# Optimization experiments

Hardware: AMD Instinct MI355X
Metric: run time of the kernel (lower is better)

Reference implementation:

```python
import jax, jax.numpy as jnp
import numpy as np

B, T_MEM, T_TGT = 32, 256, 128
E = H = 512          # embed_size == hidden_size == memory feature dim (required by module math)
V = 10000            # vocab size


def setup_inputs() -> dict:
    key = jax.random.key(0)
    ks = jax.random.split(key, 10)
    s = 0.05
    return {
        "memory": jax.random.normal(ks[0], (B, T_MEM, E), dtype=jnp.float32),
        "tgt": jax.random.randint(ks[1], (B, T_TGT), 0, V),
        "emb_in": jax.random.normal(ks[2], (V, E), dtype=jnp.float32) * s,
        "W_ih": jax.random.normal(ks[3], (4 * H, E + H), dtype=jnp.float32) * s,
        "W_hh": jax.random.normal(ks[4], (4 * H, H), dtype=jnp.float32) * s,
        "b_ih": jax.random.normal(ks[5], (4 * H,), dtype=jnp.float32) * s,
        "b_hh": jax.random.normal(ks[6], (4 * H,), dtype=jnp.float32) * s,
        "W_out": jax.random.normal(ks[7], (V, H), dtype=jnp.float32) * s,
        "b_out": jax.random.normal(ks[8], (V,), dtype=jnp.float32) * s,
    }


def reference(memory, tgt, emb_in, W_ih, W_hh, b_ih, b_hh, W_out, b_out):
    # memory: (B, T_mem, E); tgt: (B, T_tgt) int
    Bq, Tm, Ed = memory.shape
    Hd = W_hh.shape[1]
    scale = 1.0 / jnp.sqrt(jnp.asarray(Ed, dtype=memory.dtype))

    x_emb = emb_in[tgt]                       # (B, T_tgt, E) teacher-forced inputs
    x_seq = jnp.swapaxes(x_emb, 0, 1)         # (T_tgt, B, E) for scan

    def step(carry, x_t):
        h, c = carry                          # (B, H), (B, H)
        # scaled dot-product attention: query=h, keys=values=memory
        scores = jnp.einsum('be,bte->bt', h, memory) * scale
        attn = jax.nn.softmax(scores, axis=-1)
        context = jnp.einsum('bt,bte->be', attn, memory)   # (B, E)
        inp = jnp.concatenate([context, x_t], axis=-1)     # (B, E + E_embed)
        gates = inp @ W_ih.T + b_ih + h @ W_hh.T + b_hh    # (B, 4H)
        i, f, g, o = jnp.split(gates, 4, axis=-1)          # torch LSTMCell gate order
        c_new = jax.nn.sigmoid(f) * c + jax.nn.sigmoid(i) * jnp.tanh(g)
        h_new = jax.nn.sigmoid(o) * jnp.tanh(c_new)
        logits = h_new @ W_out.T + b_out                   # (B, V)
        return (h_new, c_new), logits

    h0 = jnp.zeros((Bq, Hd), dtype=memory.dtype)
    c0 = jnp.zeros((Bq, Hd), dtype=memory.dtype)
    _, logits_seq = jax.lax.scan(step, (h0, c0), x_seq)    # (T_tgt, B, V)
    return jnp.swapaxes(logits_seq, 0, 1)                  # (B, T_tgt, V)
```

## Files before the change

kernel.cpp:

```cpp
#include <hip/hip_runtime.h>
#include <stdint.h>

#define TT 128

typedef __attribute__((ext_vector_type(8))) short short8;
typedef __attribute__((ext_vector_type(4))) float f32x4;
typedef __attribute__((ext_vector_type(4))) uint32_t u32x4;

__device__ __forceinline__ float blo(uint32_t u){ union{uint32_t i; float f;} v; v.i = u << 16; return v.f; }
__device__ __forceinline__ float bhi(uint32_t u){ union{uint32_t i; float f;} v; v.i = u & 0xffff0000u; return v.f; }
__device__ __forceinline__ float bf2f(uint16_t u){ union{uint32_t i; float f;} v; v.i = ((uint32_t)u) << 16; return v.f; }
__device__ __forceinline__ uint16_t f2bf(float f){
  union{float f; uint32_t i;} v; v.f = f;
  uint32_t r = v.i + 0x7fffu + ((v.i >> 16) & 1u);
  return (uint16_t)(r >> 16);
}
__device__ __forceinline__ uint32_t bfpack(float a, float b) {
  return (uint32_t)f2bf(a) | ((uint32_t)f2bf(b) << 16);
}
__device__ __forceinline__ void xstore(uint32_t* p, uint32_t v) {
  __hip_atomic_store(p, v, __ATOMIC_RELAXED, __HIP_MEMORY_SCOPE_AGENT);
}
__device__ __forceinline__ uint32_t xload(const uint32_t* p) {
  return __hip_atomic_load(p, __ATOMIC_RELAXED, __HIP_MEMORY_SCOPE_AGENT);
}
__device__ __forceinline__ void xstore64(unsigned long long* p, unsigned long long v) {
  __hip_atomic_store(p, v, __ATOMIC_RELAXED, __HIP_MEMORY_SCOPE_AGENT);
}
__device__ __forceinline__ unsigned long long xload64(const unsigned long long* p) {
  return __hip_atomic_load(p, __ATOMIC_RELAXED, __HIP_MEMORY_SCOPE_AGENT);
}
__device__ __forceinline__ void xstoref(float* p, float v) {
  __hip_atomic_store(p, v, __ATOMIC_RELAXED, __HIP_MEMORY_SCOPE_AGENT);
}
__device__ __forceinline__ float xloadf(const float* p) {
  return __hip_atomic_load(p, __ATOMIC_RELAXED, __HIP_MEMORY_SCOPE_AGENT);
}

__global__ __launch_bounds__(256) void k_prep_mem(const float* __restrict__ mem,
                                                  uint32_t* __restrict__ memK,
                                                  uint32_t* __restrict__ memT) {
  int idx = blockIdx.x * 256 + threadIdx.x;
  if (idx < 2097152) {
    int e2 = idx & 255, k = (idx >> 8) & 255, b = idx >> 16;
    const float* p = mem + ((size_t)(b * 256 + k)) * 512 + e2 * 2;
    memK[idx] = bfpack(p[0], p[1]);
  } else {
    int j = idx - 2097152;
    int k = j & 255, e2 = (j >> 8) & 255, b = j >> 16;
    const float* p = mem + ((size_t)(b * 256 + k)) * 512 + e2 * 2;
    memT[j] = bfpack(p[0], p[1]);
  }
}

__global__ __launch_bounds__(256) void k_prep_wsl(const float* __restrict__ W_ih, const float* __restrict__ W_hh,
                                                  uint32_t* __restrict__ Wsl) {
  int idx = blockIdx.x * 256 + threadIdx.x;
  int kk = idx & 3, t = (idx >> 2) & 255, kc = (idx >> 10) & 127, s = idx >> 17;
  int j = (t & 3) * 512 + s * 64 + (t >> 2);
  int k0 = kc * 8 + kk * 2;
  float w0 = (k0 < 512) ? W_ih[(size_t)j * 1024 + k0] : W_hh[(size_t)j * 512 + (k0 - 512)];
  float w1 = (k0 + 1 < 512) ? W_ih[(size_t)j * 1024 + k0 + 1] : W_hh[(size_t)j * 512 + (k0 + 1 - 512)];
  Wsl[idx] = bfpack(w0, w1);
}

__global__ __launch_bounds__(256) void k_prep_wx(const float* __restrict__ W_ih,
                                                 const float* __restrict__ b_ih, const float* __restrict__ b_hh,
                                                 uint16_t* __restrict__ Wxp, float* __restrict__ biasp) {
  int idx = blockIdx.x * 256 + threadIdx.x;
  int k = idx & 511, j = idx >> 9;
  Wxp[idx] = f2bf(W_ih[(size_t)j * 1024 + 512 + k]);
  if (k == 0) biasp[j] = b_ih[j] + b_hh[j];
}

__global__ __launch_bounds__(256) void k_prep_wo(const float* __restrict__ W_out, uint16_t* __restrict__ WoP) {
  int idx = blockIdx.x * 256 + threadIdx.x;
  if (idx < 5120000) WoP[idx] = f2bf(W_out[idx]);
  else WoP[idx] = 0;
}

__global__ __launch_bounds__(256) void k_gather_x(const float* __restrict__ emb, const int* __restrict__ tgt,
                                                  uint16_t* __restrict__ Axg) {
  int idx = blockIdx.x * 256 + threadIdx.x;
  int k = idx & 511, m = idx >> 9;
  Axg[idx] = f2bf(emb[(size_t)tgt[m] * 512 + k]);
}

template<int MODE>
__global__ __launch_bounds__(256) void gemm_bt(const uint16_t* __restrict__ A, const uint16_t* __restrict__ B,
                                               const float* __restrict__ bias, void* __restrict__ Cout,
                                               int K, int Nreal, int ldc, int tilesN) {
  __shared__ __align__(16) uint16_t As[128 * 32];
  __shared__ __align__(16) uint16_t Bs[128 * 32];
  const int tid = threadIdx.x;
  const int wv = tid >> 6, lane = tid & 63;
  const int tm = blockIdx.x / tilesN, tn = blockIdx.x % tilesN;
  const int wr = wv >> 1, wc = wv & 1;

  f32x4 acc[4][4];
#pragma unroll
  for (int m = 0; m < 4; ++m)
#pragma unroll
    for (int n = 0; n < 4; ++n) acc[m][n] = (f32x4){0.f, 0.f, 0.f, 0.f};

  const int frow = lane & 15;
  const int fk = (lane >> 4) << 3;
  const int srow = lane >> 2;
  const int skof = (lane & 3) << 3;

  const uint16_t* Abase = A + (size_t)tm * 128 * K;
  const uint16_t* Bbase = B + (size_t)tn * 128 * K;

  for (int k0 = 0; k0 < K; k0 += 32) {
    __syncthreads();
#pragma unroll
    for (int i = 0; i < 2; ++i) {
      const int chunk = wv * 2 + i;
      const int row = chunk * 16 + srow;
      const uint16_t* ga = Abase + (size_t)row * K + k0 + skof;
      const uint16_t* gb = Bbase + (size_t)row * K + k0 + skof;
      __builtin_amdgcn_global_load_lds((const __attribute__((address_space(1))) uint32_t*)(const void*)ga,
                                       (__attribute__((address_space(3))) uint32_t*)(void*)(As + chunk * 512),
                                       16, 0, 0);
      __builtin_amdgcn_global_load_lds((const __attribute__((address_space(1))) uint32_t*)(const void*)gb,
                                       (__attribute__((address_space(3))) uint32_t*)(void*)(Bs + chunk * 512),
                                       16, 0, 0);
    }
    __syncthreads();
    short8 af[4], bfr[4];
#pragma unroll
    for (int m = 0; m < 4; ++m) af[m] = *(const short8*)(As + (wr * 64 + m * 16 + frow) * 32 + fk);
#pragma unroll
    for (int n = 0; n < 4; ++n) bfr[n] = *(const short8*)(Bs + (wc * 64 + n * 16 + frow) * 32 + fk);
#pragma unroll
    for (int m = 0; m < 4; ++m)
#pragma unroll
      for (int n = 0; n < 4; ++n)
        acc[m][n] = __builtin_amdgcn_mfma_f32_16x16x32_bf16(af[m], bfr[n], acc[m][n], 0, 0, 0);
  }

  const int crow = (lane >> 4) << 2;
  const int ccol = lane & 15;
#pragma unroll
  for (int n = 0; n < 4; ++n) {
    const int gcol = tn * 128 + wc * 64 + n * 16 + ccol;
    if (gcol < Nreal) {
      const float bv = bias[gcol];
#pragma unroll
      for (int m = 0; m < 4; ++m) {
#pragma unroll
        for (int j = 0; j < 4; ++j) {
          const int grow = tm * 128 + wr * 64 + m * 16 + crow + j;
          const float v = acc[m][n][j] + bv;
          if (MODE == 0) ((float*)Cout)[(size_t)grow * ldc + gcol] = v;
          else {
            int q = gcol >> 9, r = gcol & 511;
            int pos = ((r >> 6) << 8) + ((r & 63) << 2) + q;
            ((uint16_t*)Cout)[(size_t)grow * ldc + pos] = f2bf(v);
          }
        }
      }
    }
  }
}

__global__ __launch_bounds__(512, 1) void recur_kernel(
    const uint32_t* __restrict__ memK, const uint32_t* __restrict__ memT,
    const uint32_t* __restrict__ Wsl, const uint16_t* __restrict__ Xgp,
    unsigned long long* __restrict__ ugl, float* __restrict__ zgl,
    uint32_t* __restrict__ hgl, uint16_t* __restrict__ hA, uint32_t* __restrict__ flags) {
  __shared__ __align__(16) uint32_t mTl[8192];
  __shared__ __align__(16) uint32_t mKl[8192];
  __shared__ __align__(16) uint32_t hx[256];
  __shared__ __align__(16) float xf[1024];
  __shared__ float red[256];
  __shared__ float rux[512], ruy[512];
  __shared__ float accs[512];
  __shared__ float el[32];

  const int g = blockIdx.x;
  const int b = g >> 3, s = g & 7;
  const int tid = threadIdx.x;
  const int lane = tid & 63;
  const int wv = tid >> 6;
  const int sub = tid & 31, p = tid >> 5;
  const int row = tid & 255, half = tid >> 8;

  const uint32_t* mTb = memT + ((size_t)b << 16);
  const uint32_t* mKb = memK + ((size_t)b << 16) + ((size_t)(32 * s) << 8);
  const uint32_t* wrow = Wsl + ((size_t)s << 17) + row * 4;
  uint32_t* flagsb = flags + b * 32;
  unsigned long long* ub = ugl + ((size_t)(b << 3) << 8);

  for (int j = tid; j < 8192; j += 512) {
    mKl[j] = mKb[j];
    int e2 = j >> 5, kk = j & 31;
    mTl[j] = mTb[e2 * 256 + 32 * s + kk];
  }

  float c = 0.f;
  if (tid < 256) hx[tid] = 0u;
  xf[tid] = 0.f; xf[512 + tid] = 0.f;
  __syncthreads();

  for (int t = 0; t < TT; ++t) {
    {
      float sc = 0.f;
#pragma unroll
      for (int i = 0; i < 16; ++i) {
        uint32_t mw = mTl[(p + (i << 4)) * 32 + sub];
        uint32_t hw = hx[p + (i << 4)];
        sc = fmaf(blo(mw), blo(hw), sc);
        sc = fmaf(bhi(mw), bhi(hw), sc);
      }
      sc += __shfl_xor(sc, 32);
      if (lane < 32) red[wv * 32 + lane] = sc;
    }
    __syncthreads();
    if (tid < 32) {
      float sf = red[tid] + red[32 + tid] + red[64 + tid] + red[96 + tid]
               + red[128 + tid] + red[160 + tid] + red[192 + tid] + red[224 + tid];
      float e = __expf(sf * 0.044194173824159216f);
      el[tid] = e;
      float z = e;
      z += __shfl_xor(z, 16); z += __shfl_xor(z, 8);
      z += __shfl_xor(z, 4);  z += __shfl_xor(z, 2); z += __shfl_xor(z, 1);
      if (tid == 0) xstoref(&zgl[(b << 3) + s], z);
    }
    __syncthreads();
    {
      float ux = 0.f, uy = 0.f;
      const int k0 = half * 16;
#pragma unroll
      for (int kk = 0; kk < 16; ++kk) {
        uint32_t mw = mKl[(k0 + kk) * 256 + row];
        float e = el[k0 + kk];
        ux = fmaf(blo(mw), e, ux);
        uy = fmaf(bhi(mw), e, uy);
      }
      rux[tid] = ux; ruy[tid] = uy;
    }
    __syncthreads();
    if (tid < 256) {
      union { float f[2]; unsigned long long u; } pk;
      pk.f[0] = rux[tid] + rux[tid + 256];
      pk.f[1] = ruy[tid] + ruy[tid + 256];
      xstore64(&ub[(s << 8) + tid], pk.u);
    }
    __syncthreads();
    if (tid == 0) xstore(&flagsb[s], (uint32_t)(2 * t + 1));
    float acc = (half == 0) ? bf2f(Xgp[((size_t)b * TT + t) * 2048 + (s << 8) + row]) : 0.f;
    {
      const int kcb = 64 + 32 * half;
#pragma unroll 8
      for (int j = 0; j < 32; ++j) {
        const int kc = kcb + j;
        u32x4 w4 = *(const u32x4*)(wrow + kc * 1024);
        f32x4 xa = *(const f32x4*)(xf + kc * 8);
        f32x4 xb = *(const f32x4*)(xf + kc * 8 + 4);
        acc = fmaf(blo(w4.x), xa.x, acc); acc = fmaf(bhi(w4.x), xa.y, acc);
        acc = fmaf(blo(w4.y), xa.z, acc); acc = fmaf(bhi(w4.y), xa.w, acc);
        acc = fmaf(blo(w4.z), xb.x, acc); acc = fmaf(bhi(w4.z), xb.y, acc);
        acc = fmaf(blo(w4.w), xb.z, acc); acc = fmaf(bhi(w4.w), xb.w, acc);
      }
    }
    if (tid < 64) {
      int v;
      do {
        __builtin_amdgcn_s_sleep(2);
        v = (tid < 8) ? (int)xload(&flagsb[tid]) : (2 * t + 1);
      } while (__any(v < 2 * t + 1));
    }
    __syncthreads();
    {
      float zsum = 0.f;
      if (tid < 256) {
#pragma unroll
        for (int q = 0; q < 8; ++q) zsum += xloadf(&zgl[(b << 3) + q]);
      }
      float ux = 0.f, uy = 0.f;
      const int q0 = half * 4;
#pragma unroll
      for (int q = 0; q < 4; ++q) {
        union { float f[2]; unsigned long long u; } pk;
        pk.u = xload64(&ub[((q0 + q) << 8) + row]);
        ux += pk.f[0]; uy += pk.f[1];
      }
      rux[tid] = ux; ruy[tid] = uy;
      __syncthreads();
      if (tid < 256) {
        float rz = 1.f / zsum;
        xf[2 * tid]     = (rux[tid] + rux[tid + 256]) * rz;
        xf[2 * tid + 1] = (ruy[tid] + ruy[tid + 256]) * rz;
      }
    }
    __syncthreads();
    {
      const int kcb = 32 * half;
#pragma unroll 8
      for (int j = 0; j < 32; ++j) {
        const int kc = kcb + j;
        u32x4 w4 = *(const u32x4*)(wrow + kc * 1024);
        f32x4 xa = *(const f32x4*)(xf + kc * 8);
        f32x4 xb = *(const f32x4*)(xf + kc * 8 + 4);
        acc = fmaf(blo(w4.x), xa.x, acc); acc = fmaf(bhi(w4.x), xa.y, acc);
        acc = fmaf(blo(w4.y), xa.z, acc); acc = fmaf(bhi(w4.y), xa.w, acc);
        acc = fmaf(blo(w4.z), xb.x, acc); acc = fmaf(bhi(w4.z), xb.y, acc);
        acc = fmaf(blo(w4.w), xb.z, acc); acc = fmaf(bhi(w4.w), xb.w, acc);
      }
      accs[tid] = acc;
    }
    __syncthreads();
    if (tid < 256) {
      float tot = accs[tid] + accs[tid + 256];
      int lbase = lane & ~3;
      float gi = __shfl(tot, lbase, 64);
      float gf = __shfl(tot, lbase + 1, 64);
      float gg = __shfl(tot, lbase + 2, 64);
      float go = __shfl(tot, lbase + 3, 64);
      c = (1.f / (1.f + __expf(-gf))) * c + (1.f / (1.f + __expf(-gi))) * tanhf(gg);
      float hn = (1.f / (1.f + __expf(-go))) * tanhf(c);
      float hn4 = __shfl(hn, (lane & ~7) + 4, 64);
      if ((tid & 7) == 0) {
        uint32_t hp = bfpack(hn, hn4);
        int r2 = (s << 5) + (tid >> 3);
        xstore(&hgl[(b << 8) + r2], hp);
        ((uint32_t*)hA)[((size_t)b * TT + t) * 256 + r2] = hp;
      }
    }
    __syncthreads();
    if (tid == 0) xstore(&flagsb[s], (uint32_t)(2 * t + 2));
    if (tid < 64) {
      int v;
      do {
        __builtin_amdgcn_s_sleep(2);
        v = (tid < 8) ? (int)xload(&flagsb[tid]) : (2 * t + 2);
      } while (__any(v < 2 * t + 2));
    }
    __syncthreads();
    if (tid < 256) {
      uint32_t hp = xload(&hgl[(b << 8) + tid]);
      hx[tid] = hp;
      xf[512 + 2 * tid] = blo(hp);
      xf[513 + 2 * tid] = bhi(hp);
    }
    __syncthreads();
  }
}

extern "C" void kernel_launch(void* const* d_in, const int* in_sizes, int n_in,
                              void* d_out, int out_size, void* d_ws, size_t ws_size,
                              hipStream_t stream) {
  const float* memory = (const float*)d_in[0];
  const int*   tgt    = (const int*)d_in[1];
  const float* emb_in = (const float*)d_in[2];
  const float* W_ih   = (const float*)d_in[3];
  const float* W_hh   = (const float*)d_in[4];
  const float* b_ih   = (const float*)d_in[5];
  const float* b_hh   = (const float*)d_in[6];
  const float* W_out  = (const float*)d_in[7];
  const float* b_out  = (const float*)d_in[8];
  float* out = (float*)d_out;
  char* ws = (char*)d_ws;

  uint32_t* memK  = (uint32_t*)(ws);
  uint32_t* memT  = (uint32_t*)(ws + 8388608);
  uint32_t* Wsl   = (uint32_t*)(ws + 16777216);
  uint16_t* Wxp   = (uint16_t*)(ws + 20971520);
  float*    biasp = (float*)(ws + 23068672);
  uint16_t* WoP   = (uint16_t*)(ws + 23076864);
  uint16_t* Axg   = (uint16_t*)(ws + 33431552);
  uint16_t* Xgp   = (uint16_t*)(ws + 37625856);
  uint16_t* hA    = (uint16_t*)(ws + 54403072);
  uint32_t* hgl   = (uint32_t*)(ws + 58597376);
  float*    zgl   = (float*)(ws + 58630144);
  uint32_t* flags = (uint32_t*)(ws + 58662912);
  unsigned long long* ugl = (unsigned long long*)Axg;

  hipMemsetAsync(flags, 0, 4096, stream);

  k_prep_mem<<<16384, 256, 0, stream>>>(memory, memK, memT);
  k_prep_wsl<<<4096, 256, 0, stream>>>(W_ih, W_hh, Wsl);
  k_prep_wx<<<4096, 256, 0, stream>>>(W_ih, b_ih, b_hh, Wxp, biasp);
  k_prep_wo<<<20224, 256, 0, stream>>>(W_out, WoP);
  k_gather_x<<<8192, 256, 0, stream>>>(emb_in, tgt, Axg);

  gemm_bt<1><<<32 * 16, 256, 0, stream>>>(Axg, Wxp, biasp, Xgp, 512, 2048, 2048, 16);

  recur_kernel<<<256, 512, 0, stream>>>(memK, memT, Wsl, Xgp, ugl, zgl, hgl, hA, flags);

  gemm_bt<0><<<32 * 79, 256, 0, stream>>>(hA, WoP, b_out, out, 512, 10000, 10000, 79);
}
```

Baseline: 1.907 ms.

## Process two batch rows per recurrent block and halve the recurrence grid

Each block of the persistent recurrence kernel now owns the same hidden slice for two batch rows (b and b+16). Both rows' memory tiles are staged in doubled shared-memory buffers, and the grid shrinks from 256 to 128 blocks. Per step, the attention phase runs for both rows before any cross-block wait, so one row's flag wait can overlap the other row's work. In exchange, each block does twice the serial work per step with more barriers, and it uses much more LDS. The hidden-state part of the gate matvec is no longer computed before the spin-wait, which removes an existing overlap.

```diff
diff --git a/kernel.cpp b/kernel.cpp
--- a/kernel.cpp
+++ b/kernel.cpp
@@ -169,180 +169,180 @@
     const uint32_t* __restrict__ Wsl, const uint16_t* __restrict__ Xgp,
     unsigned long long* __restrict__ ugl, float* __restrict__ zgl,
     uint32_t* __restrict__ hgl, uint16_t* __restrict__ hA, uint32_t* __restrict__ flags) {
-  __shared__ __align__(16) uint32_t mTl[8192];
-  __shared__ __align__(16) uint32_t mKl[8192];
-  __shared__ __align__(16) uint32_t hx[256];
-  __shared__ __align__(16) float xf[1024];
+  __shared__ __align__(16) uint32_t mTl[2][8192];
+  __shared__ __align__(16) uint32_t mKl[2][8192];
+  __shared__ __align__(16) uint32_t hx[2][256];
+  __shared__ __align__(16) float xf[2][1024];
   __shared__ float red[256];
   __shared__ float rux[512], ruy[512];
   __shared__ float accs[512];
   __shared__ float el[32];
 
   const int g = blockIdx.x;
-  const int b = g >> 3, s = g & 7;
+  const int s = g & 7, pp = g >> 3;
   const int tid = threadIdx.x;
   const int lane = tid & 63;
   const int wv = tid >> 6;
   const int sub = tid & 31, p = tid >> 5;
   const int row = tid & 255, half = tid >> 8;
 
-  const uint32_t* mTb = memT + ((size_t)b << 16);
-  const uint32_t* mKb = memK + ((size_t)b << 16) + ((size_t)(32 * s) << 8);
   const uint32_t* wrow = Wsl + ((size_t)s << 17) + row * 4;
-  uint32_t* flagsb = flags + b * 32;
-  unsigned long long* ub = ugl + ((size_t)(b << 3) << 8);
-
-  for (int j = tid; j < 8192; j += 512) {
-    mKl[j] = mKb[j];
-    int e2 = j >> 5, kk = j & 31;
-    mTl[j] = mTb[e2 * 256 + 32 * s + kk];
-  }
-
-  float c = 0.f;
-  if (tid < 256) hx[tid] = 0u;
-  xf[tid] = 0.f; xf[512 + tid] = 0.f;
+
+#pragma unroll
+  for (int bi = 0; bi < 2; ++bi) {
+    const int b = pp + bi * 16;
+    const uint32_t* mTb = memT + ((size_t)b << 16);
+    const uint32_t* mKb = memK + ((size_t)b << 16) + ((size_t)(32 * s) << 8);
+    for (int j = tid; j < 8192; j += 512) {
+      mKl[bi][j] = mKb[j];
+      int e2 = j >> 5, kk = j & 31;
+      mTl[bi][j] = mTb[e2 * 256 + 32 * s + kk];
+    }
+  }
+  float c[2] = {0.f, 0.f};
+  if (tid < 256) { hx[0][tid] = 0u; hx[1][tid] = 0u; }
+  xf[0][tid] = 0.f; xf[0][512 + tid] = 0.f;
+  xf[1][tid] = 0.f; xf[1][512 + tid] = 0.f;
   __syncthreads();
 
   for (int t = 0; t < TT; ++t) {
-    {
-      float sc = 0.f;
-#pragma unroll
-      for (int i = 0; i < 16; ++i) {
-        uint32_t mw = mTl[(p + (i << 4)) * 32 + sub];
-        uint32_t hw = hx[p + (i << 4)];
-        sc = fmaf(blo(mw), blo(hw), sc);
-        sc = fmaf(bhi(mw), bhi(hw), sc);
-      }
-      sc += __shfl_xor(sc, 32);
-      if (lane < 32) red[wv * 32 + lane] = sc;
-    }
-    __syncthreads();
-    if (tid < 32) {
-      float sf = red[tid] + red[32 + tid] + red[64 + tid] + red[96 + tid]
-               + red[128 + tid] + red[160 + tid] + red[192 + tid] + red[224 + tid];
-      float e = __expf(sf * 0.044194173824159216f);
-      el[tid] = e;
-      float z = e;
-      z += __shfl_xor(z, 16); z += __shfl_xor(z, 8);
-      z += __shfl_xor(z, 4);  z += __shfl_xor(z, 2); z += __shfl_xor(z, 1);
-      if (tid == 0) xstoref(&zgl[(b << 3) + s], z);
-    }
-    __syncthreads();
-    {
-      float ux = 0.f, uy = 0.f;
-      const int k0 = half * 16;
-#pragma unroll
-      for (int kk = 0; kk < 16; ++kk) {
-        uint32_t mw = mKl[(k0 + kk) * 256 + row];
-        float e = el[k0 + kk];
-        ux = fmaf(blo(mw), e, ux);
-        uy = fmaf(bhi(mw), e, uy);
-      }
-      rux[tid] = ux; ruy[tid] = uy;
-    }
-    __syncthreads();
-    if (tid < 256) {
-      union { float f[2]; unsigned long long u; } pk;
-      pk.f[0] = rux[tid] + rux[tid + 256];
-      pk.f[1] = ruy[tid] + ruy[tid + 256];
-      xstore64(&ub[(s << 8) + tid], pk.u);
-    }
-    __syncthreads();
-    if (tid == 0) xstore(&flagsb[s], (uint32_t)(2 * t + 1));
-    float acc = (half == 0) ? bf2f(Xgp[((size_t)b * TT + t) * 2048 + (s << 8) + row]) : 0.f;
-    {
-      const int kcb = 64 + 32 * half;
+#pragma unroll
+    for (int bi = 0; bi < 2; ++bi) {
+      const int b = pp + bi * 16;
+      {
+        float sc = 0.f;
+#pragma unroll
+        for (int i = 0; i < 16; ++i) {
+          uint32_t mw = mTl[bi][(p + (i << 4)) * 32 + sub];
+          uint32_t hw = hx[bi][p + (i << 4)];
+          sc = fmaf(blo(mw), blo(hw), sc);
+          sc = fmaf(bhi(mw), bhi(hw), sc);
+        }
+        sc += __shfl_xor(sc, 32);
+        if (lane < 32) red[wv * 32 + lane] = sc;
+      }
+      __syncthreads();
+      if (tid < 32) {
+        float sf = red[tid] + red[32 + tid] + red[64 + tid] + red[96 + tid]
+                 + red[128 + tid] + red[160 + tid] + red[192 + tid] + red[224 + tid];
+        float e = __expf(sf * 0.044194173824159216f);
+        el[tid] = e;
+        float z = e;
+        z += __shfl_xor(z, 16); z += __shfl_xor(z, 8);
+        z += __shfl_xor(z, 4);  z += __shfl_xor(z, 2); z += __shfl_xor(z, 1);
+        if (tid == 0) xstoref(&zgl[(b << 3) + s], z);
+      }
+      __syncthreads();
+      {
+        float ux = 0.f, uy = 0.f;
+        const int k0 = half * 16;
+#pragma unroll
+        for (int kk = 0; kk < 16; ++kk) {
+          uint32_t mw = mKl[bi][(k0 + kk) * 256 + row];
+          float e = el[k0 + kk];
+          ux = fmaf(blo(mw), e, ux);
+          uy = fmaf(bhi(mw), e, uy);
+        }
+        rux[tid] = ux; ruy[tid] = uy;
+      }
+      __syncthreads();
+      if (tid < 256) {
+        union { float f[2]; unsigned long long u; } pk;
+        pk.f[0] = rux[tid] + rux[tid + 256];
+        pk.f[1] = ruy[tid] + ruy[tid + 256];
+        xstore64(&ugl[(((size_t)b << 3) + s << 8) + tid], pk.u);
+      }
+      __syncthreads();
+      if (tid == 0) xstore(&flags[b * 32 + s], (uint32_t)(2 * t + 1));
+    }
+#pragma unroll
+    for (int bi = 0; bi < 2; ++bi) {
+      const int b = pp + bi * 16;
+      if (tid < 64) {
+        int v;
+        do {
+          __builtin_amdgcn_s_sleep(2);
+          v = (tid < 8) ? (int)xload(&flags[b * 32 + tid]) : (2 * t + 1);
+        } while (__any(v < 2 * t + 1));
+      }
+      __syncthreads();
+      {
+        float zsum = 0.f;
+        if (tid < 256) {
+#pragma unroll
+          for (int q = 0; q < 8; ++q) zsum += xloadf(&zgl[(b << 3) + q]);
+        }
+        float ux = 0.f, uy = 0.f;
+        const int q0 = half * 4;
+#pragma unroll
+        for (int q = 0; q < 4; ++q) {
+          union { float f[2]; unsigned long long u; } pk;
+          pk.u = xload64(&ugl[(((size_t)b << 3) + (q0 + q) << 8) + row]);
+          ux += pk.f[0]; uy += pk.f[1];
+        }
+        rux[tid] = ux; ruy[tid] = uy;
+        __syncthreads();
+        if (tid < 256) {
+          float rz = 1.f / zsum;
+          xf[bi][2 * tid]     = (rux[tid] + rux[tid + 256]) * rz;
+          xf[bi][2 * tid + 1] = (ruy[tid] + ruy[tid + 256]) * rz;
+        }
+      }
+      __syncthreads();
+      {
+        float acc = (half == 0) ? bf2f(Xgp[((size_t)b * TT + t) * 2048 + (s << 8) + row]) : 0.f;
+        const int kcb = half * 64;
 #pragma unroll 8
-      for (int j = 0; j < 32; ++j) {
-        const int kc = kcb + j;
-        u32x4 w4 = *(const u32x4*)(wrow + kc * 1024);
-        f32x4 xa = *(const f32x4*)(xf + kc * 8);
-        f32x4 xb = *(const f32x4*)(xf + kc * 8 + 4);
-        acc = fmaf(blo(w4.x), xa.x, acc); acc = fmaf(bhi(w4.x), xa.y, acc);
-        acc = fmaf(blo(w4.y), xa.z, acc); acc = fmaf(bhi(w4.y), xa.w, acc);
-        acc = fmaf(blo(w4.z), xb.x, acc); acc = fmaf(bhi(w4.z), xb.y, acc);
-        acc = fmaf(blo(w4.w), xb.z, acc); acc = fmaf(bhi(w4.w), xb.w, acc);
-      }
-    }
-    if (tid < 64) {
-      int v;
-      do {
-        __builtin_amdgcn_s_sleep(2);
-        v = (tid < 8) ? (int)xload(&flagsb[tid]) : (2 * t + 1);
-      } while (__any(v < 2 * t + 1));
-    }
-    __syncthreads();
-    {
-      float zsum = 0.f;
+        for (int j = 0; j < 64; ++j) {
+          const int kc = kcb + j;
+          u32x4 w4 = *(const u32x4*)(wrow + kc * 1024);
+          f32x4 xa = *(const f32x4*)(xf[bi] + kc * 8);
+          f32x4 xb = *(const f32x4*)(xf[bi] + kc * 8 + 4);
+          acc = fmaf(blo(w4.x), xa.x, acc); acc = fmaf(bhi(w4.x), xa.y, acc);
+          acc = fmaf(blo(w4.y), xa.z, acc); acc = fmaf(bhi(w4.y), xa.w, acc);
+          acc = fmaf(blo(w4.z), xb.x, acc); acc = fmaf(bhi(w4.z), xb.y, acc);
+          acc = fmaf(blo(w4.w), xb.z, acc); acc = fmaf(bhi(w4.w), xb.w, acc);
+        }
+        accs[tid] = acc;
+      }
+      __syncthreads();
       if (tid < 256) {
-#pragma unroll
-        for (int q = 0; q < 8; ++q) zsum += xloadf(&zgl[(b << 3) + q]);
-      }
-      float ux = 0.f, uy = 0.f;
-      const int q0 = half * 4;
-#pragma unroll
-      for (int q = 0; q < 4; ++q) {
-        union { float f[2]; unsigned long long u; } pk;
-        pk.u = xload64(&ub[((q0 + q) << 8) + row]);
-        ux += pk.f[0]; uy += pk.f[1];
-      }
-      rux[tid] = ux; ruy[tid] = uy;
+        float tot = accs[tid] + accs[tid + 256];
+        int lbase = lane & ~3;
+        float gi = __shfl(tot, lbase, 64);
+        float gf = __shfl(tot, lbase + 1, 64);
+        float gg = __shfl(tot, lbase + 2, 64);
+        float go = __shfl(tot, lbase + 3, 64);
+        c[bi] = (1.f / (1.f + __expf(-gf))) * c[bi] + (1.f / (1.f + __expf(-gi))) * tanhf(gg);
+        float hn = (1.f / (1.f + __expf(-go))) * tanhf(c[bi]);
+        float hn4 = __shfl(hn, (lane & ~7) + 4, 64);
+        if ((tid & 7) == 0) {
+          uint32_t hp = bfpack(hn, hn4);
+          int r2 = (s << 5) + (tid >> 3);
+          xstore(&hgl[(b << 8) + r2], hp);
+          ((uint32_t*)hA)[((size_t)b * TT + t) * 256 + r2] = hp;
+        }
+      }
+      __syncthreads();
+      if (tid == 0) xstore(&flags[b * 32 + s], (uint32_t)(2 * t + 2));
+    }
+#pragma unroll
+    for (int bi = 0; bi < 2; ++bi) {
+      const int b = pp + bi * 16;
+      if (tid < 64) {
+        int v;
+        do {
+          __builtin_amdgcn_s_sleep(2);
+          v = (tid < 8) ? (int)xload(&flags[b * 32 + tid]) : (2 * t + 2);
+        } while (__any(v < 2 * t + 2));
+      }
       __syncthreads();
       if (tid < 256) {
-        float rz = 1.f / zsum;
-        xf[2 * tid]     = (rux[tid] + rux[tid + 256]) * rz;
-        xf[2 * tid + 1] = (ruy[tid] + ruy[tid + 256]) * rz;
-      }
-    }
-    __syncthreads();
-    {
-      const int kcb = 32 * half;
-#pragma unroll 8
-      for (int j = 0; j < 32; ++j) {
-        const int kc = kcb + j;
-        u32x4 w4 = *(const u32x4*)(wrow + kc * 1024);
-        f32x4 xa = *(const f32x4*)(xf + kc * 8);
-        f32x4 xb = *(const f32x4*)(xf + kc * 8 + 4);
-        acc = fmaf(blo(w4.x), xa.x, acc); acc = fmaf(bhi(w4.x), xa.y, acc);
-        acc = fmaf(blo(w4.y), xa.z, acc); acc = fmaf(bhi(w4.y), xa.w, acc);
-        acc = fmaf(blo(w4.z), xb.x, acc); acc = fmaf(bhi(w4.z), xb.y, acc);
-        acc = fmaf(blo(w4.w), xb.z, acc); acc = fmaf(bhi(w4.w), xb.w, acc);
-      }
-      accs[tid] = acc;
-    }
-    __syncthreads();
-    if (tid < 256) {
-      float tot = accs[tid] + accs[tid + 256];
-      int lbase = lane & ~3;
-      float gi = __shfl(tot, lbase, 64);
-      float gf = __shfl(tot, lbase + 1, 64);
-      float gg = __shfl(tot, lbase + 2, 64);
-      float go = __shfl(tot, lbase + 3, 64);
-      c = (1.f / (1.f + __expf(-gf))) * c + (1.f / (1.f + __expf(-gi))) * tanhf(gg);
-      float hn = (1.f / (1.f + __expf(-go))) * tanhf(c);
-      float hn4 = __shfl(hn, (lane & ~7) + 4, 64);
-      if ((tid & 7) == 0) {
-        uint32_t hp = bfpack(hn, hn4);
-        int r2 = (s << 5) + (tid >> 3);
-        xstore(&hgl[(b << 8) + r2], hp);
-        ((uint32_t*)hA)[((size_t)b * TT + t) * 256 + r2] = hp;
-      }
-    }
-    __syncthreads();
-    if (tid == 0) xstore(&flagsb[s], (uint32_t)(2 * t + 2));
-    if (tid < 64) {
-      int v;
-      do {
-        __builtin_amdgcn_s_sleep(2);
-        v = (tid < 8) ? (int)xload(&flagsb[tid]) : (2 * t + 2);
-      } while (__any(v < 2 * t + 2));
-    }
-    __syncthreads();
-    if (tid < 256) {
-      uint32_t hp = xload(&hgl[(b << 8) + tid]);
-      hx[tid] = hp;
-      xf[512 + 2 * tid] = blo(hp);
-      xf[513 + 2 * tid] = bhi(hp);
+        uint32_t hp = xload(&hgl[(b << 8) + tid]);
+        hx[bi][tid] = hp;
+        xf[bi][512 + 2 * tid] = blo(hp);
+        xf[bi][513 + 2 * tid] = bhi(hp);
+      }
     }
     __syncthreads();
   }
@@ -387,7 +387,7 @@
 
   gemm_bt<1><<<32 * 16, 256, 0, stream>>>(Axg, Wxp, biasp, Xgp, 512, 2048, 2048, 16);
 
-  recur_kernel<<<256, 512, 0, stream>>>(memK, memT, Wsl, Xgp, ugl, zgl, hgl, hA, flags);
+  recur_kernel<<<128, 512, 0, stream>>>(memK, memT, Wsl, Xgp, ugl, zgl, hgl, hA, flags);
 
   gemm_bt<0><<<32 * 79, 256, 0, stream>>>(hA, WoP, b_out, out, 512, 10000, 10000, 79);
 }
```

After: 2.127 ms. 1.12x slower.
